# Optimization experiments

Hardware: AMD Instinct MI355X
Metric: run time of the kernel (lower is better)

Reference implementation:

```python
import jax, jax.numpy as jnp
import numpy as np

B = 128   # num graphs
N_PER = 64  # nodes per graph
E = 65536   # real edges
K = 16      # emb_dim (poly feature width)
D = 64      # out_dim


def _all_pairs_index(num_graphs, n):
    # dense per-graph all-pairs edge index, row-major (coalesce sorted order)
    off = jnp.arange(num_graphs, dtype=jnp.int64) * n          # [B]
    rr = jnp.repeat(jnp.arange(n, dtype=jnp.int64), n)          # [n*n]
    cc = jnp.tile(jnp.arange(n, dtype=jnp.int64), n)            # [n*n]
    rows = (off[:, None] + rr[None, :]).reshape(-1)             # [B*n*n]
    cols = (off[:, None] + cc[None, :]).reshape(-1)
    return jnp.stack([rows, cols])                              # [2, B*n*n]


def setup_inputs() -> dict:
    key = jax.random.key(0)
    k0, k1, k2, k3, k4 = jax.random.split(key, 5)
    poly_idx = _all_pairs_index(B, N_PER)                       # dense poly PE indices
    poly_val = jax.random.normal(k0, (B * N_PER * N_PER, K), dtype=jnp.float32)
    g = jax.random.randint(k1, (E,), 0, B)
    lr = jax.random.randint(k2, (E,), 0, N_PER)
    lc = jax.random.randint(k3, (E,), 0, N_PER)
    edge_index = jnp.stack([g * N_PER + lr, g * N_PER + lc]).astype(jnp.int64)
    edge_attr = jax.random.normal(k4, (E, D), dtype=jnp.float32)
    # xavier_uniform for fc.weight [D, K]
    bound = float(np.sqrt(6.0 / (K + D)))
    W = jax.random.uniform(jax.random.fold_in(key, 7), (D, K), dtype=jnp.float32,
                           minval=-bound, maxval=bound)
    batch = jnp.repeat(jnp.arange(B, dtype=jnp.int64), N_PER)   # [N]
    return {"poly_val": poly_val, "edge_attr": edge_attr, "W": W,
            "poly_idx": poly_idx, "edge_index": edge_index,
            "batch": batch, "num_graphs": B}


def reference(poly_val, edge_attr, W, poly_idx, edge_index, batch, num_graphs):
    N = batch.shape[0]
    n = N // num_graphs                 # equal-sized graphs
    e_full = num_graphs * n * n
    d = W.shape[0]

    # poly_val = fc(poly_val)  (no bias)
    pv = poly_val @ W.T                 # [Np, D]

    # coalesce over concat([edge_index, poly_idx, full_edge_index]) with op='add'.
    # Since every (within-graph) edge is a member of the all-pairs set, the
    # coalesced index is exactly full_edge_index in row-major sorted order;
    # values are scatter-added into their all-pairs slot. The fill_value=0
    # padding for full_edge_index contributes zeros.
    def slot(idx):
        r, c = idx[0], idx[1]
        g = r // n
        return g * (n * n) + (r % n) * n + (c % n)

    out_val = jnp.zeros((e_full, d), dtype=pv.dtype)
    out_val = out_val.at[slot(edge_index)].add(edge_attr)
    out_val = out_val.at[slot(poly_idx)].add(pv)

    full_edge_index = _all_pairs_index(num_graphs, n)
    return full_edge_index, out_val
```

## Files before the change

kernel.cpp:

```cpp
#include <hip/hip_runtime.h>

#define EF      524288
#define NEDGE   65536
#define KDIM    16
#define DDIM    64
#define TPW     4
#define PVBLK   (EF / (32 * TPW) / 4)
#define LSTR    68
#define NTILE   (EF / 32)
#define CAP     64
#define PF      8

typedef float vfloat4 __attribute__((ext_vector_type(4)));
typedef short bf16x8  __attribute__((ext_vector_type(8)));
typedef float f32x16  __attribute__((ext_vector_type(16)));

__device__ __forceinline__ short f2bf(float f) {
    unsigned u = __float_as_uint(f);
    return (short)((u + 0x7FFFu + ((u >> 16) & 1u)) >> 16);
}

__device__ __forceinline__ long edge_slot(const int* ei, int e) {
    int r = ei[e];
    int c = ei[NEDGE + e];
    return ((long)(r >> 6) << 12) + ((long)(r & 63) << 6) + (long)(c & 63);
}

#define WS_CNT_OFF   0
#define WS_LIST_OFF  (64 * 1024)
#define WS_OVFC_OFF  (WS_LIST_OFF + NTILE * CAP * 4)
#define WS_OVFL_OFF  (WS_OVFC_OFF + 4)
#define WS_NEED      (WS_OVFL_OFF + NEDGE * 4)

__global__ __launch_bounds__(256) void zero_cnt(unsigned* __restrict__ cnt,
                                                unsigned* __restrict__ ovfc) {
    int gid = blockIdx.x * 256 + threadIdx.x;
    cnt[gid] = 0u;
    if (gid == 0) *ovfc = 0u;
}

__global__ __launch_bounds__(256) void bin_edges(const int* __restrict__ ei,
                                                 unsigned* __restrict__ cnt,
                                                 int* __restrict__ list,
                                                 unsigned* __restrict__ ovfc,
                                                 int* __restrict__ ovfl) {
    int e = blockIdx.x * 256 + threadIdx.x;
    long slot = edge_slot(ei, e);
    int tile = (int)(slot >> 5);
    int row  = (int)(slot & 31);
    unsigned pos = atomicAdd(&cnt[tile], 1u);
    if (pos < CAP) list[tile * CAP + pos] = (e << 5) | row;
    else           ovfl[atomicAdd(ovfc, 1u)] = e;
}

__global__ __launch_bounds__(256) void pv_fused(const float* __restrict__ pv,
                                                const float* __restrict__ W,
                                                const float* __restrict__ ea,
                                                const unsigned* __restrict__ cnt,
                                                const int* __restrict__ list,
                                                float* __restrict__ out,
                                                float* __restrict__ outv) {
    __shared__ float lds[4][32 * LSTR];
    int tid = threadIdx.x;
    int wv  = tid >> 6;
    int l   = tid & 63;
    int n   = l & 31;
    int kh  = l >> 5;
    long j0 = ((long)blockIdx.x * 4 + wv) * (32 * TPW);
    int tile0 = (int)(j0 >> 5);

    unsigned ec[TPW];
#pragma unroll
    for (int tt = 0; tt < TPW; ++tt) ec[tt] = cnt[tile0 + tt];

    int pk[TPW][PF];
#pragma unroll
    for (int tt = 0; tt < TPW; ++tt)
#pragma unroll
        for (int i = 0; i < PF; ++i)
            pk[tt][i] = list[(long)(tile0 + tt) * CAP + i];

    {
        int jb = blockIdx.x * 512;
#pragma unroll
        for (int r = 0; r < 2; ++r) {
            int j = jb + r * 256 + tid;
            int g = j >> 12;
            int rem = j & 4095;
            out[j]      = (float)((g << 6) + (rem >> 6));
            out[EF + j] = (float)((g << 6) + (rem & 63));
        }
    }

    float vpre[TPW][PF];
#pragma unroll
    for (int tt = 0; tt < TPW; ++tt)
#pragma unroll
        for (int i = 0; i < PF; ++i) {
            unsigned e = ((unsigned)pk[tt][i] >> 5) & (NEDGE - 1);
            vpre[tt][i] = ea[(long)e * DDIM + l];
        }

    unsigned ep[TPW];
#pragma unroll
    for (int tt = 0; tt < TPW; ++tt) {
        if (ec[tt] > CAP) ec[tt] = CAP;
        ep[tt] = ec[tt] > PF ? PF : ec[tt];
    }

    float4 ba[TPW], bb[TPW];
#pragma unroll
    for (int tt = 0; tt < TPW; ++tt) {
        const float4* bp = reinterpret_cast<const float4*>(pv + (j0 + tt * 32 + n) * KDIM + kh * 8);
        ba[tt] = bp[0]; bb[tt] = bp[1];
    }

    const float4* wp0 = reinterpret_cast<const float4*>(W + n * KDIM + kh * 8);
    const float4* wp1 = reinterpret_cast<const float4*>(W + (32 + n) * KDIM + kh * 8);
    float4 w0a = wp0[0], w0b = wp0[1], w1a = wp1[0], w1b = wp1[1];
    bf16x8 xa0, xa1;
    xa0[0]=f2bf(w0a.x); xa0[1]=f2bf(w0a.y); xa0[2]=f2bf(w0a.z); xa0[3]=f2bf(w0a.w);
    xa0[4]=f2bf(w0b.x); xa0[5]=f2bf(w0b.y); xa0[6]=f2bf(w0b.z); xa0[7]=f2bf(w0b.w);
    xa1[0]=f2bf(w1a.x); xa1[1]=f2bf(w1a.y); xa1[2]=f2bf(w1a.z); xa1[3]=f2bf(w1a.w);
    xa1[4]=f2bf(w1b.x); xa1[5]=f2bf(w1b.y); xa1[6]=f2bf(w1b.z); xa1[7]=f2bf(w1b.w);

    float* myl = lds[wv];

#pragma unroll
    for (int tt = 0; tt < TPW; ++tt) {
        long jt = j0 + tt * 32;
        bf16x8 yf;
        yf[0]=f2bf(ba[tt].x); yf[1]=f2bf(ba[tt].y); yf[2]=f2bf(ba[tt].z); yf[3]=f2bf(ba[tt].w);
        yf[4]=f2bf(bb[tt].x); yf[5]=f2bf(bb[tt].y); yf[6]=f2bf(bb[tt].z); yf[7]=f2bf(bb[tt].w);
        f32x16 acc0 = {0,0,0,0, 0,0,0,0, 0,0,0,0, 0,0,0,0};
        f32x16 acc1 = {0,0,0,0, 0,0,0,0, 0,0,0,0, 0,0,0,0};
        acc0 = __builtin_amdgcn_mfma_f32_32x32x16_bf16(xa0, yf, acc0, 0, 0, 0);
        acc1 = __builtin_amdgcn_mfma_f32_32x32x16_bf16(xa1, yf, acc1, 0, 0, 0);
#pragma unroll
        for (int q = 0; q < 4; ++q) {
            vfloat4 s0 = {acc0[4*q], acc0[4*q+1], acc0[4*q+2], acc0[4*q+3]};
            vfloat4 s1 = {acc1[4*q], acc1[4*q+1], acc1[4*q+2], acc1[4*q+3]};
            *reinterpret_cast<vfloat4*>(myl + n * LSTR + 8*q + 4*kh)      = s0;
            *reinterpret_cast<vfloat4*>(myl + n * LSTR + 32 + 8*q + 4*kh) = s1;
        }
#pragma unroll
        for (int i = 0; i < PF; ++i)
            if ((unsigned)i < ep[tt]) myl[(pk[tt][i] & 31) * LSTR + l] += vpre[tt][i];
        for (unsigned i = PF; i < ec[tt]; ++i) {
            int packed = list[(long)(tile0 + tt) * CAP + i];
            myl[(packed & 31) * LSTR + l] += ea[(long)(packed >> 5) * DDIM + l];
        }
#pragma unroll
        for (int i = 0; i < 8; ++i) {
            int row  = 4*i + (l >> 4);
            int colf = (l & 15) * 4;
            vfloat4 v = *reinterpret_cast<const vfloat4*>(myl + row * LSTR + colf);
            *reinterpret_cast<vfloat4*>(outv + (jt + row) * DDIM + colf) = v;
        }
    }
}

__global__ __launch_bounds__(256) void ovf_fix(const float* __restrict__ ea,
                                               const int* __restrict__ ei,
                                               const unsigned* __restrict__ ovfc,
                                               const int* __restrict__ ovfl,
                                               float* __restrict__ outv) {
    unsigned nov = *ovfc;
    for (unsigned i = blockIdx.x * 256 + threadIdx.x; i < nov; i += 4 * 256) {
        int e = ovfl[i];
        long slot = edge_slot(ei, e);
        float* dst = outv + slot * DDIM;
        const float* src = ea + (long)e * DDIM;
        for (int j = 0; j < DDIM; ++j) unsafeAtomicAdd(dst + j, src[j]);
    }
}

__global__ __launch_bounds__(256) void pv_gemm(const float* __restrict__ pv,
                                               const float* __restrict__ W,
                                               float* __restrict__ outv) {
    __shared__ float lds[4][32 * LSTR];
    int tid = threadIdx.x;
    int wv  = tid >> 6;
    int l   = tid & 63;
    int n   = l & 31;
    int kh  = l >> 5;
    long j0 = ((long)blockIdx.x * 4 + wv) * 64;

    const float4* wp0 = reinterpret_cast<const float4*>(W + n * KDIM + kh * 8);
    const float4* wp1 = reinterpret_cast<const float4*>(W + (32 + n) * KDIM + kh * 8);
    float4 w0a = wp0[0], w0b = wp0[1], w1a = wp1[0], w1b = wp1[1];
    bf16x8 xa0, xa1;
    xa0[0]=f2bf(w0a.x); xa0[1]=f2bf(w0a.y); xa0[2]=f2bf(w0a.z); xa0[3]=f2bf(w0a.w);
    xa0[4]=f2bf(w0b.x); xa0[5]=f2bf(w0b.y); xa0[6]=f2bf(w0b.z); xa0[7]=f2bf(w0b.w);
    xa1[0]=f2bf(w1a.x); xa1[1]=f2bf(w1a.y); xa1[2]=f2bf(w1a.z); xa1[3]=f2bf(w1a.w);
    xa1[4]=f2bf(w1b.x); xa1[5]=f2bf(w1b.y); xa1[6]=f2bf(w1b.z); xa1[7]=f2bf(w1b.w);

    float* myl = lds[wv];
#pragma unroll
    for (int t = 0; t < 2; ++t) {
        long jt = j0 + t * 32;
        const float4* bp = reinterpret_cast<const float4*>(pv + (jt + n) * KDIM + kh * 8);
        float4 ba = bp[0], bb = bp[1];
        bf16x8 yf;
        yf[0]=f2bf(ba.x); yf[1]=f2bf(ba.y); yf[2]=f2bf(ba.z); yf[3]=f2bf(ba.w);
        yf[4]=f2bf(bb.x); yf[5]=f2bf(bb.y); yf[6]=f2bf(bb.z); yf[7]=f2bf(bb.w);

        f32x16 acc0 = {0,0,0,0, 0,0,0,0, 0,0,0,0, 0,0,0,0};
        f32x16 acc1 = {0,0,0,0, 0,0,0,0, 0,0,0,0, 0,0,0,0};
        acc0 = __builtin_amdgcn_mfma_f32_32x32x16_bf16(xa0, yf, acc0, 0, 0, 0);
        acc1 = __builtin_amdgcn_mfma_f32_32x32x16_bf16(xa1, yf, acc1, 0, 0, 0);
#pragma unroll
        for (int q = 0; q < 4; ++q) {
            vfloat4 s0 = {acc0[4*q], acc0[4*q+1], acc0[4*q+2], acc0[4*q+3]};
            vfloat4 s1 = {acc1[4*q], acc1[4*q+1], acc1[4*q+2], acc1[4*q+3]};
            *reinterpret_cast<vfloat4*>(myl + n * LSTR + 8*q + 4*kh)      = s0;
            *reinterpret_cast<vfloat4*>(myl + n * LSTR + 32 + 8*q + 4*kh) = s1;
        }
#pragma unroll
        for (int i = 0; i < 8; ++i) {
            int row  = 4*i + (l >> 4);
            int colf = (l & 15) * 4;
            vfloat4 v = *reinterpret_cast<const vfloat4*>(myl + row * LSTR + colf);
            *reinterpret_cast<vfloat4*>(outv + (jt + row) * DDIM + colf) = v;
        }
    }
}

__global__ __launch_bounds__(256) void fill_idx_plain(float* __restrict__ out) {
    int gid = blockIdx.x * 256 + threadIdx.x;
    int j0 = gid << 2;
    vfloat4 rv, cv;
#pragma unroll
    for (int i = 0; i < 4; ++i) {
        int j = j0 + i;
        int g = j >> 12;
        int rem = j & 4095;
        rv[i] = (float)((g << 6) + (rem >> 6));
        cv[i] = (float)((g << 6) + (rem & 63));
    }
    *reinterpret_cast<vfloat4*>(out + j0)      = rv;
    *reinterpret_cast<vfloat4*>(out + EF + j0) = cv;
}

__global__ __launch_bounds__(256) void scatter_edges(const float* __restrict__ ea,
                                                     const int* __restrict__ ei,
                                                     float* __restrict__ outv) {
    int gid = blockIdx.x * 256 + threadIdx.x;
    int e = gid >> 4;
    int t = gid & 15;
    long slot = edge_slot(ei, e);
    float4 v = *reinterpret_cast<const float4*>(ea + (long)e * DDIM + t * 4);
    float* dst = outv + slot * DDIM + t * 4;
    unsafeAtomicAdd(dst + 0, v.x);
    unsafeAtomicAdd(dst + 1, v.y);
    unsafeAtomicAdd(dst + 2, v.z);
    unsafeAtomicAdd(dst + 3, v.w);
}

extern "C" void kernel_launch(void* const* d_in, const int* in_sizes, int n_in,
                              void* d_out, int out_size, void* d_ws, size_t ws_size,
                              hipStream_t stream) {
    const float* poly_val  = (const float*)d_in[0];
    const float* edge_attr = (const float*)d_in[1];
    const float* W         = (const float*)d_in[2];
    const int*   edge_index = (const int*)d_in[4];

    float* out  = (float*)d_out;
    float* outv = out + 2 * (long)EF;

    if (ws_size >= (size_t)WS_NEED) {
        char* ws = (char*)d_ws;
        unsigned* cnt  = (unsigned*)(ws + WS_CNT_OFF);
        int*      list = (int*)     (ws + WS_LIST_OFF);
        unsigned* ovfc = (unsigned*)(ws + WS_OVFC_OFF);
        int*      ovfl = (int*)     (ws + WS_OVFL_OFF);

        zero_cnt<<<NTILE / 256, 256, 0, stream>>>(cnt, ovfc);
        bin_edges<<<NEDGE / 256, 256, 0, stream>>>(edge_index, cnt, list, ovfc, ovfl);
        pv_fused<<<PVBLK, 256, 0, stream>>>(poly_val, W, edge_attr, cnt, list, out, outv);
        ovf_fix<<<4, 256, 0, stream>>>(edge_attr, edge_index, ovfc, ovfl, outv);
    } else {
        fill_idx_plain<<<EF / 4 / 256, 256, 0, stream>>>(out);
        pv_gemm<<<EF / 64 / 4, 256, 0, stream>>>(poly_val, W, outv);
        scatter_edges<<<(NEDGE * 16) / 256, 256, 0, stream>>>(edge_attr, edge_index, outv);
    }
}
```

Before: 45.76 us.

## Accumulate edge rows into MFMA registers and store directly, dropping LDS staging

Replaces the LDS-staged fused kernel with a register-only version. The matching lane adds each binned edge's attribute row straight into the MFMA accumulator fragments, and the result is written to global memory from the MFMA output layout. Tiles per wave drop from 4 to 2, which doubles the block count. This removes the LDS write, read-modify-write and read round trip, but it gives up the prefetched edge loads and makes the per-edge loop divergent, since only one lane pair does the adds and the edge loads are dependent. Stores become row-strided 16-byte chunks instead of fully coalesced rows.

```diff
diff --git a/kernel.cpp b/kernel.cpp
--- a/kernel.cpp
+++ b/kernel.cpp
@@ -4,9 +4,8 @@
 #define NEDGE   65536
 #define KDIM    16
 #define DDIM    64
-#define TPW     4
+#define TPW     2
 #define PVBLK   (EF / (32 * TPW) / 4)
-#define LSTR    68
 #define NTILE   (EF / 32)
 #define CAP     64
 #define PF      8
@@ -53,14 +52,13 @@
     else           ovfl[atomicAdd(ovfc, 1u)] = e;
 }
 
-__global__ __launch_bounds__(256) void pv_fused(const float* __restrict__ pv,
-                                                const float* __restrict__ W,
-                                                const float* __restrict__ ea,
-                                                const unsigned* __restrict__ cnt,
-                                                const int* __restrict__ list,
-                                                float* __restrict__ out,
-                                                float* __restrict__ outv) {
-    __shared__ float lds[4][32 * LSTR];
+__global__ __launch_bounds__(256) void pv_fused_reg(const float* __restrict__ pv,
+                                                    const float* __restrict__ W,
+                                                    const float* __restrict__ ea,
+                                                    const unsigned* __restrict__ cnt,
+                                                    const int* __restrict__ list,
+                                                    float* __restrict__ out,
+                                                    float* __restrict__ outv) {
     int tid = threadIdx.x;
     int wv  = tid >> 6;
     int l   = tid & 63;
@@ -69,51 +67,26 @@
     long j0 = ((long)blockIdx.x * 4 + wv) * (32 * TPW);
     int tile0 = (int)(j0 >> 5);
 
-    unsigned ec[TPW];
-#pragma unroll
-    for (int tt = 0; tt < TPW; ++tt) ec[tt] = cnt[tile0 + tt];
-
-    int pk[TPW][PF];
-#pragma unroll
-    for (int tt = 0; tt < TPW; ++tt)
-#pragma unroll
-        for (int i = 0; i < PF; ++i)
-            pk[tt][i] = list[(long)(tile0 + tt) * CAP + i];
+    unsigned ec0 = cnt[tile0];
+    unsigned ec1 = cnt[tile0 + 1];
+    int pk0[PF], pk1[PF];
+#pragma unroll
+    for (int i = 0; i < PF; ++i) {
+        pk0[i] = list[(long)tile0 * CAP + i];
+        pk1[i] = list[(long)(tile0 + 1) * CAP + i];
+    }
 
     {
-        int jb = blockIdx.x * 512;
-#pragma unroll
-        for (int r = 0; r < 2; ++r) {
-            int j = jb + r * 256 + tid;
-            int g = j >> 12;
-            int rem = j & 4095;
-            out[j]      = (float)((g << 6) + (rem >> 6));
-            out[EF + j] = (float)((g << 6) + (rem & 63));
-        }
-    }
-
-    float vpre[TPW][PF];
-#pragma unroll
-    for (int tt = 0; tt < TPW; ++tt)
-#pragma unroll
-        for (int i = 0; i < PF; ++i) {
-            unsigned e = ((unsigned)pk[tt][i] >> 5) & (NEDGE - 1);
-            vpre[tt][i] = ea[(long)e * DDIM + l];
-        }
-
-    unsigned ep[TPW];
-#pragma unroll
-    for (int tt = 0; tt < TPW; ++tt) {
-        if (ec[tt] > CAP) ec[tt] = CAP;
-        ep[tt] = ec[tt] > PF ? PF : ec[tt];
-    }
-
-    float4 ba[TPW], bb[TPW];
-#pragma unroll
-    for (int tt = 0; tt < TPW; ++tt) {
-        const float4* bp = reinterpret_cast<const float4*>(pv + (j0 + tt * 32 + n) * KDIM + kh * 8);
-        ba[tt] = bp[0]; bb[tt] = bp[1];
-    }
+        int j = blockIdx.x * 256 + tid;
+        int g = j >> 12;
+        int rem = j & 4095;
+        out[j]      = (float)((g << 6) + (rem >> 6));
+        out[EF + j] = (float)((g << 6) + (rem & 63));
+    }
+
+    const float4* bp0 = reinterpret_cast<const float4*>(pv + (j0 + n) * KDIM + kh * 8);
+    const float4* bp1 = reinterpret_cast<const float4*>(pv + (j0 + 32 + n) * KDIM + kh * 8);
+    float4 ba0 = bp0[0], bb0 = bp0[1], ba1 = bp1[0], bb1 = bp1[1];
 
     const float4* wp0 = reinterpret_cast<const float4*>(W + n * KDIM + kh * 8);
     const float4* wp1 = reinterpret_cast<const float4*>(W + (32 + n) * KDIM + kh * 8);
@@ -124,38 +97,52 @@
     xa1[0]=f2bf(w1a.x); xa1[1]=f2bf(w1a.y); xa1[2]=f2bf(w1a.z); xa1[3]=f2bf(w1a.w);
     xa1[4]=f2bf(w1b.x); xa1[5]=f2bf(w1b.y); xa1[6]=f2bf(w1b.z); xa1[7]=f2bf(w1b.w);
 
-    float* myl = lds[wv];
+    unsigned ecc0 = ec0 > CAP ? CAP : ec0;
+    unsigned ecc1 = ec1 > CAP ? CAP : ec1;
 
 #pragma unroll
     for (int tt = 0; tt < TPW; ++tt) {
         long jt = j0 + tt * 32;
+        float4 ba = tt ? ba1 : ba0;
+        float4 bb = tt ? bb1 : bb0;
+        unsigned ec = tt ? ecc1 : ecc0;
+        int tile = tile0 + tt;
+
         bf16x8 yf;
-        yf[0]=f2bf(ba[tt].x); yf[1]=f2bf(ba[tt].y); yf[2]=f2bf(ba[tt].z); yf[3]=f2bf(ba[tt].w);
-        yf[4]=f2bf(bb[tt].x); yf[5]=f2bf(bb[tt].y); yf[6]=f2bf(bb[tt].z); yf[7]=f2bf(bb[tt].w);
+        yf[0]=f2bf(ba.x); yf[1]=f2bf(ba.y); yf[2]=f2bf(ba.z); yf[3]=f2bf(ba.w);
+        yf[4]=f2bf(bb.x); yf[5]=f2bf(bb.y); yf[6]=f2bf(bb.z); yf[7]=f2bf(bb.w);
+
         f32x16 acc0 = {0,0,0,0, 0,0,0,0, 0,0,0,0, 0,0,0,0};
         f32x16 acc1 = {0,0,0,0, 0,0,0,0, 0,0,0,0, 0,0,0,0};
         acc0 = __builtin_amdgcn_mfma_f32_32x32x16_bf16(xa0, yf, acc0, 0, 0, 0);
         acc1 = __builtin_amdgcn_mfma_f32_32x32x16_bf16(xa1, yf, acc1, 0, 0, 0);
+
+        for (unsigned i = 0; i < ec; ++i) {
+            int packed = (i < PF) ? (tt ? pk1[i] : pk0[i])
+                                  : list[(long)tile * CAP + i];
+            int row = packed & 31;
+            if (n == row) {
+                long eb = (long)(packed >> 5) * DDIM;
+                const float4* er = reinterpret_cast<const float4*>(ea + eb + kh * 4);
+#pragma unroll
+                for (int q = 0; q < 4; ++q) {
+                    float4 e0 = er[2*q];
+                    float4 e1 = er[2*q + 8];
+                    acc0[4*q]   += e0.x; acc0[4*q+1] += e0.y;
+                    acc0[4*q+2] += e0.z; acc0[4*q+3] += e0.w;
+                    acc1[4*q]   += e1.x; acc1[4*q+1] += e1.y;
+                    acc1[4*q+2] += e1.z; acc1[4*q+3] += e1.w;
+                }
+            }
+        }
+
+        float* base = outv + (jt + n) * DDIM + kh * 4;
 #pragma unroll
         for (int q = 0; q < 4; ++q) {
             vfloat4 s0 = {acc0[4*q], acc0[4*q+1], acc0[4*q+2], acc0[4*q+3]};
             vfloat4 s1 = {acc1[4*q], acc1[4*q+1], acc1[4*q+2], acc1[4*q+3]};
-            *reinterpret_cast<vfloat4*>(myl + n * LSTR + 8*q + 4*kh)      = s0;
-            *reinterpret_cast<vfloat4*>(myl + n * LSTR + 32 + 8*q + 4*kh) = s1;
-        }
-#pragma unroll
-        for (int i = 0; i < PF; ++i)
-            if ((unsigned)i < ep[tt]) myl[(pk[tt][i] & 31) * LSTR + l] += vpre[tt][i];
-        for (unsigned i = PF; i < ec[tt]; ++i) {
-            int packed = list[(long)(tile0 + tt) * CAP + i];
-            myl[(packed & 31) * LSTR + l] += ea[(long)(packed >> 5) * DDIM + l];
-        }
-#pragma unroll
-        for (int i = 0; i < 8; ++i) {
-            int row  = 4*i + (l >> 4);
-            int colf = (l & 15) * 4;
-            vfloat4 v = *reinterpret_cast<const vfloat4*>(myl + row * LSTR + colf);
-            *reinterpret_cast<vfloat4*>(outv + (jt + row) * DDIM + colf) = v;
+            *reinterpret_cast<vfloat4*>(base + 8*q)      = s0;
+            *reinterpret_cast<vfloat4*>(base + 8*q + 32) = s1;
         }
     }
 }
@@ -178,7 +165,6 @@
 __global__ __launch_bounds__(256) void pv_gemm(const float* __restrict__ pv,
                                                const float* __restrict__ W,
                                                float* __restrict__ outv) {
-    __shared__ float lds[4][32 * LSTR];
     int tid = threadIdx.x;
     int wv  = tid >> 6;
     int l   = tid & 63;
@@ -195,7 +181,6 @@
     xa1[0]=f2bf(w1a.x); xa1[1]=f2bf(w1a.y); xa1[2]=f2bf(w1a.z); xa1[3]=f2bf(w1a.w);
     xa1[4]=f2bf(w1b.x); xa1[5]=f2bf(w1b.y); xa1[6]=f2bf(w1b.z); xa1[7]=f2bf(w1b.w);
 
-    float* myl = lds[wv];
 #pragma unroll
     for (int t = 0; t < 2; ++t) {
         long jt = j0 + t * 32;
@@ -209,19 +194,14 @@
         f32x16 acc1 = {0,0,0,0, 0,0,0,0, 0,0,0,0, 0,0,0,0};
         acc0 = __builtin_amdgcn_mfma_f32_32x32x16_bf16(xa0, yf, acc0, 0, 0, 0);
         acc1 = __builtin_amdgcn_mfma_f32_32x32x16_bf16(xa1, yf, acc1, 0, 0, 0);
+
+        float* base = outv + (jt + n) * DDIM + kh * 4;
 #pragma unroll
         for (int q = 0; q < 4; ++q) {
             vfloat4 s0 = {acc0[4*q], acc0[4*q+1], acc0[4*q+2], acc0[4*q+3]};
             vfloat4 s1 = {acc1[4*q], acc1[4*q+1], acc1[4*q+2], acc1[4*q+3]};
-            *reinterpret_cast<vfloat4*>(myl + n * LSTR + 8*q + 4*kh)      = s0;
-            *reinterpret_cast<vfloat4*>(myl + n * LSTR + 32 + 8*q + 4*kh) = s1;
-        }
-#pragma unroll
-        for (int i = 0; i < 8; ++i) {
-            int row  = 4*i + (l >> 4);
-            int colf = (l & 15) * 4;
-            vfloat4 v = *reinterpret_cast<const vfloat4*>(myl + row * LSTR + colf);
-            *reinterpret_cast<vfloat4*>(outv + (jt + row) * DDIM + colf) = v;
+            *reinterpret_cast<vfloat4*>(base + 8*q)      = s0;
+            *reinterpret_cast<vfloat4*>(base + 8*q + 32) = s1;
         }
     }
 }
@@ -277,11 +257,11 @@
 
         zero_cnt<<<NTILE / 256, 256, 0, stream>>>(cnt, ovfc);
         bin_edges<<<NEDGE / 256, 256, 0, stream>>>(edge_index, cnt, list, ovfc, ovfl);
-        pv_fused<<<PVBLK, 256, 0, stream>>>(poly_val, W, edge_attr, cnt, list, out, outv);
+        pv_fused_reg<<<PVBLK, 256, 0, stream>>>(poly_val, W, edge_attr, cnt, list, out, outv);
         ovf_fix<<<4, 256, 0, stream>>>(edge_attr, edge_index, ovfc, ovfl, outv);
     } else {
         fill_idx_plain<<<EF / 4 / 256, 256, 0, stream>>>(out);
-        pv_gemm<<<EF / 64 / 4, 256, 0, stream>>>(poly_val, W, outv);
+        pv_gemm<<<EF / 256, 256, 0, stream>>>(poly_val, W, outv);
         scatter_edges<<<(NEDGE * 16) / 256, 256, 0, stream>>>(edge_attr, edge_index, outv);
     }
 }
```

After: 73.49 us. 60.6% more time.
